# Kernel tuning notes

Measured on AMD Instinct MI355X. Metric: run time of the kernel, lower is better.

Reference implementation:

```python
import jax, jax.numpy as jnp
import numpy as np

N, D = 8192, 64


def setup_inputs() -> dict:
    key = jax.random.key(0)
    k1, k2, k3 = jax.random.split(key, 3)
    X = jax.random.normal(k1, (N, D), dtype=jnp.float32)
    target = jax.random.normal(k2, (N,), dtype=jnp.float32)
    params = jax.random.uniform(k3, (D,), dtype=jnp.float32)  # positive ARD weights
    return {"X": X, "target": target, "params": params}


def reference(X, target, params):
    # ARD-RBF kernel: k(x, y) = exp(-sum(params * (x - y)^2))
    # = exp(-||xs - ys||^2) with xs = x * sqrt(params)
    Xs = X * jnp.sqrt(params)  # [N, D]
    sq = jnp.sum(Xs * Xs, axis=-1)  # [N]
    d2 = jnp.maximum(sq[:, None] + sq[None, :] - 2.0 * (Xs @ Xs.T), 0.0)  # [N, N]
    K = jnp.exp(-d2)
    # torch version initializes K = eye(N) and never overwrites the diagonal
    n = X.shape[0]
    K = K.at[jnp.arange(n), jnp.arange(n)].set(1.0)
    K_target = jnp.outer(target, target)  # [N, N]
    kta = jnp.sum(K * K_target) / (n * jnp.sqrt(jnp.sum(K * K)))
    return -kta
```

## Files before the change

### kernel.cpp

```cpp
#include <hip/hip_runtime.h>
#include <hip/hip_bf16.h>

#define NROWS 8192
#define DIM 64
#define NT 64
#define NTRI (NT * (NT + 1) / 2)

typedef __attribute__((ext_vector_type(8))) short short8;
typedef __attribute__((ext_vector_type(4))) float f32x4;

static constexpr float LOG2E = 1.4426950408889634f;

#if defined(__has_builtin) && __has_builtin(__builtin_amdgcn_exp2f)
#define EXP2F(x) __builtin_amdgcn_exp2f(x)
#else
#define EXP2F(x) exp2f(x)
#endif

__global__ __launch_bounds__(256) void prep_kernel(const float* __restrict__ X,
                                                   const float* __restrict__ params,
                                                   float* __restrict__ Lsq,
                                                   short* __restrict__ Xp) {
    int tid  = threadIdx.x;
    int wave = tid >> 6, lane = tid & 63;
    int r8 = lane >> 3, c = lane & 7;
    int row = blockIdx.x * 32 + wave * 8 + r8;

    const float* xr = X + row * DIM + c * 8;
    float4 x0 = *(const float4*)xr;
    float4 x1 = *(const float4*)(xr + 4);
    float4 p0 = *(const float4*)(params + c * 8);
    float4 p1 = *(const float4*)(params + c * 8 + 4);

    float v[8];
    v[0] = x0.x * sqrtf(p0.x); v[1] = x0.y * sqrtf(p0.y);
    v[2] = x0.z * sqrtf(p0.z); v[3] = x0.w * sqrtf(p0.w);
    v[4] = x1.x * sqrtf(p1.x); v[5] = x1.y * sqrtf(p1.y);
    v[6] = x1.z * sqrtf(p1.z); v[7] = x1.w * sqrtf(p1.w);

    short8 h;
    float s = 0.f;
    #pragma unroll
    for (int i = 0; i < 8; ++i) {
        __hip_bfloat16 b = __float2bfloat16(v[i]);
        union { __hip_bfloat16 bb; short ss; } u; u.bb = b;
        h[i] = u.ss;
        float bf = __bfloat162float(b);
        s += bf * bf;
    }

    int panel = row >> 4, pr = row & 15;
    ((short8*)Xp)[panel * 128 + c * 16 + pr] = h;

    #pragma unroll
    for (int m = 1; m < 8; m <<= 1) s += __shfl_xor(s, m, 64);
    if (c == 0) Lsq[row] = LOG2E * s;
}

__global__ __launch_bounds__(256, 3) void kta_main(const short* __restrict__ Xp,
                                                   const float* __restrict__ Lsq,
                                                   const float* __restrict__ t,
                                                   float2* __restrict__ partial) {
    int k = blockIdx.x;
    int it = (int)((129.0f - sqrtf(16641.0f - 8.0f * (float)k)) * 0.5f);
    if (it > NT - 1) it = NT - 1;
    while ((it * (129 - it)) / 2 > k) --it;
    while (((it + 1) * (128 - it)) / 2 <= k) ++it;
    int jt = it + (k - (it * (129 - it)) / 2);

    int tid  = threadIdx.x;
    int wave = tid >> 6, lane = tid & 63;
    int quad = lane >> 4, l16 = lane & 15;

    __shared__ short8 As[1024];
    __shared__ short8 Bs[1024];

    const short8* Xpv  = (const short8*)Xp;
    const short8* Asrc = Xpv + (size_t)it * 1024;
    const short8* Bsrc = Xpv + (size_t)jt * 1024;

    #pragma unroll
    for (int i = 0; i < 4; ++i) {
        As[tid + i * 256] = Asrc[tid + i * 256];
        Bs[tid + i * 256] = Bsrc[tid + i * 256];
    }

    int rbase = it * 128 + (wave >> 1) * 64;
    int cbase = jt * 128 + (wave & 1) * 64;

    float LsqR[4][4], tR[4][4];
    #pragma unroll
    for (int rt = 0; rt < 4; ++rt)
        #pragma unroll
        for (int r = 0; r < 4; ++r) {
            int row = rbase + rt * 16 + quad * 4 + r;
            LsqR[rt][r] = Lsq[row];
            tR[rt][r]   = t[row];
        }
    float LsqC[4], tC[4];
    #pragma unroll
    for (int ct = 0; ct < 4; ++ct) {
        int col = cbase + ct * 16 + l16;
        LsqC[ct] = Lsq[col];
        tC[ct]   = t[col];
    }

    __syncthreads();

    int lpA = (wave >> 1) * 4;
    int lpB = (wave & 1) * 4;

    short8 bfr[4][2];
    #pragma unroll
    for (int ct = 0; ct < 4; ++ct)
        #pragma unroll
        for (int kc = 0; kc < 2; ++kc)
            bfr[ct][kc] = Bs[(lpB + ct) * 128 + (kc * 4 + quad) * 16 + l16];

    bool diagwave = (it == jt) && ((wave >> 1) == (wave & 1));
    float s1 = 0.f, s2a = 0.f, s2b = 0.f;

    auto body = [&](int DIAG) {
        #pragma unroll
        for (int rt = 0; rt < 4; ++rt) {
            short8 a0 = As[(lpA + rt) * 128 + quad * 16 + l16];
            short8 a1 = As[(lpA + rt) * 128 + (4 + quad) * 16 + l16];
            f32x4 cc[4];
            #pragma unroll
            for (int ct = 0; ct < 4; ++ct) {
                cc[ct] = (f32x4){0.f, 0.f, 0.f, 0.f};
                cc[ct] = __builtin_amdgcn_mfma_f32_16x16x32_bf16(a0, bfr[ct][0], cc[ct], 0, 0, 0);
                cc[ct] = __builtin_amdgcn_mfma_f32_16x16x32_bf16(a1, bfr[ct][1], cc[ct], 0, 0, 0);
            }
            #pragma unroll
            for (int r = 0; r < 4; ++r) {
                float nr = LsqR[rt][r];
                float s1row = 0.f;
                #pragma unroll
                for (int ct = 0; ct < 4; ++ct) {
                    float dot = cc[ct][r];
                    float K = EXP2F(fmaf(dot, 2.0f * LOG2E, -(nr + LsqC[ct])));
                    if (DIAG && (rt == ct) && ((quad * 4 + r) == l16))
                        K = 1.0f;
                    s1row = fmaf(K, tC[ct], s1row);
                    if (ct & 2) s2b = fmaf(K, K, s2b);
                    else        s2a = fmaf(K, K, s2a);
                }
                s1 = fmaf(s1row, tR[rt][r], s1);
            }
        }
    };
    if (diagwave) body(1); else body(0);

    float s2 = s2a + s2b;
    float w = (it == jt) ? 1.0f : 2.0f;
    s1 *= w; s2 *= w;
    #pragma unroll
    for (int m = 32; m > 0; m >>= 1) {
        s1 += __shfl_xor(s1, m, 64);
        s2 += __shfl_xor(s2, m, 64);
    }

    __shared__ float2 red[4];
    if (lane == 0) red[wave] = make_float2(s1, s2);
    __syncthreads();
    if (tid == 0) {
        float2 a = red[0], b = red[1], cc = red[2], d = red[3];
        partial[k] = make_float2(a.x + b.x + cc.x + d.x, a.y + b.y + cc.y + d.y);
    }
}

__global__ __launch_bounds__(256) void finalize_kernel(const float2* __restrict__ partial,
                                                       float* __restrict__ out) {
    float s1 = 0.f, s2 = 0.f;
    for (int i = threadIdx.x; i < NTRI; i += 256) {
        float2 p = partial[i];
        s1 += p.x;
        s2 += p.y;
    }
    #pragma unroll
    for (int m = 32; m > 0; m >>= 1) {
        s1 += __shfl_xor(s1, m, 64);
        s2 += __shfl_xor(s2, m, 64);
    }
    __shared__ float r1[4], r2[4];
    int wave = threadIdx.x >> 6, lane = threadIdx.x & 63;
    if (lane == 0) { r1[wave] = s1; r2[wave] = s2; }
    __syncthreads();
    if (threadIdx.x == 0) {
        float a = r1[0] + r1[1] + r1[2] + r1[3];
        float b = r2[0] + r2[1] + r2[2] + r2[3];
        out[0] = -a / ((float)NROWS * sqrtf(b));
    }
}

extern "C" void kernel_launch(void* const* d_in, const int* in_sizes, int n_in,
                              void* d_out, int out_size, void* d_ws, size_t ws_size,
                              hipStream_t stream) {
    const float* X      = (const float*)d_in[0];
    const float* target = (const float*)d_in[1];
    const float* params = (const float*)d_in[2];
    float* out = (float*)d_out;

    float* ws = (float*)d_ws;
    float2* partial = (float2*)ws;
    float* Lsq = ws + 8192;
    short* Xp  = (short*)(ws + 16384);

    prep_kernel<<<NROWS / 32, 256, 0, stream>>>(X, params, Lsq, Xp);
    kta_main<<<NTRI, 256, 0, stream>>>(Xp, Lsq, target, partial);
    finalize_kernel<<<1, 256, 0, stream>>>(partial, out);
}
```

Before: 74.88 us.

## Fuse prep kernel into main kernel by staging scaled bf16 tiles in-block

```diff
diff --git a/kernel.cpp b/kernel.cpp
--- a/kernel.cpp
+++ b/kernel.cpp
@@ -17,48 +17,8 @@
 #define EXP2F(x) exp2f(x)
 #endif
 
-__global__ __launch_bounds__(256) void prep_kernel(const float* __restrict__ X,
+__global__ __launch_bounds__(256, 3) void kta_main(const float* __restrict__ X,
                                                    const float* __restrict__ params,
-                                                   float* __restrict__ Lsq,
-                                                   short* __restrict__ Xp) {
-    int tid  = threadIdx.x;
-    int wave = tid >> 6, lane = tid & 63;
-    int r8 = lane >> 3, c = lane & 7;
-    int row = blockIdx.x * 32 + wave * 8 + r8;
-
-    const float* xr = X + row * DIM + c * 8;
-    float4 x0 = *(const float4*)xr;
-    float4 x1 = *(const float4*)(xr + 4);
-    float4 p0 = *(const float4*)(params + c * 8);
-    float4 p1 = *(const float4*)(params + c * 8 + 4);
-
-    float v[8];
-    v[0] = x0.x * sqrtf(p0.x); v[1] = x0.y * sqrtf(p0.y);
-    v[2] = x0.z * sqrtf(p0.z); v[3] = x0.w * sqrtf(p0.w);
-    v[4] = x1.x * sqrtf(p1.x); v[5] = x1.y * sqrtf(p1.y);
-    v[6] = x1.z * sqrtf(p1.z); v[7] = x1.w * sqrtf(p1.w);
-
-    short8 h;
-    float s = 0.f;
-    #pragma unroll
-    for (int i = 0; i < 8; ++i) {
-        __hip_bfloat16 b = __float2bfloat16(v[i]);
-        union { __hip_bfloat16 bb; short ss; } u; u.bb = b;
-        h[i] = u.ss;
-        float bf = __bfloat162float(b);
-        s += bf * bf;
-    }
-
-    int panel = row >> 4, pr = row & 15;
-    ((short8*)Xp)[panel * 128 + c * 16 + pr] = h;
-
-    #pragma unroll
-    for (int m = 1; m < 8; m <<= 1) s += __shfl_xor(s, m, 64);
-    if (c == 0) Lsq[row] = LOG2E * s;
-}
-
-__global__ __launch_bounds__(256, 3) void kta_main(const short* __restrict__ Xp,
-                                                   const float* __restrict__ Lsq,
                                                    const float* __restrict__ t,
                                                    float2* __restrict__ partial) {
     int k = blockIdx.x;
@@ -71,53 +31,92 @@
     int tid  = threadIdx.x;
     int wave = tid >> 6, lane = tid & 63;
     int quad = lane >> 4, l16 = lane & 15;
+    int r8 = lane >> 3, ch = lane & 7;
 
     __shared__ short8 As[1024];
     __shared__ short8 Bs[1024];
-
-    const short8* Xpv  = (const short8*)Xp;
-    const short8* Asrc = Xpv + (size_t)it * 1024;
-    const short8* Bsrc = Xpv + (size_t)jt * 1024;
-
-    #pragma unroll
-    for (int i = 0; i < 4; ++i) {
-        As[tid + i * 256] = Asrc[tid + i * 256];
-        Bs[tid + i * 256] = Bsrc[tid + i * 256];
-    }
+    __shared__ float  LA[128];
+    __shared__ float  LB[128];
+
+    float4 p0 = *(const float4*)(params + ch * 8);
+    float4 p1 = *(const float4*)(params + ch * 8 + 4);
+    float sp[8];
+    sp[0] = sqrtf(p0.x); sp[1] = sqrtf(p0.y); sp[2] = sqrtf(p0.z); sp[3] = sqrtf(p0.w);
+    sp[4] = sqrtf(p1.x); sp[5] = sqrtf(p1.y); sp[6] = sqrtf(p1.z); sp[7] = sqrtf(p1.w);
+
+    auto stage = [&](int rowbase, short8* __restrict__ S, float* __restrict__ L) {
+        #pragma unroll
+        for (int pass = 0; pass < 4; ++pass) {
+            int rl = pass * 32 + wave * 8 + r8;
+            const float* xr = X + (size_t)(rowbase + rl) * DIM + ch * 8;
+            float4 x0 = *(const float4*)xr;
+            float4 x1 = *(const float4*)(xr + 4);
+            float v[8];
+            v[0] = x0.x * sp[0]; v[1] = x0.y * sp[1];
+            v[2] = x0.z * sp[2]; v[3] = x0.w * sp[3];
+            v[4] = x1.x * sp[4]; v[5] = x1.y * sp[5];
+            v[6] = x1.z * sp[6]; v[7] = x1.w * sp[7];
+            short8 h;
+            float s = 0.f;
+            #pragma unroll
+            for (int i = 0; i < 8; ++i) {
+                __hip_bfloat16 b = __float2bfloat16(v[i]);
+                union { __hip_bfloat16 bb; short ss; } u; u.bb = b;
+                h[i] = u.ss;
+                float bf = __bfloat162float(b);
+                s = fmaf(bf, bf, s);
+            }
+            S[(rl >> 4) * 128 + ch * 16 + (rl & 15)] = h;
+            #pragma unroll
+            for (int m = 1; m < 8; m <<= 1) s += __shfl_xor(s, m, 64);
+            if (ch == 0) L[rl] = LOG2E * s;
+        }
+    };
+
+    bool diag = (it == jt);
+    stage(it * 128, As, LA);
+    if (!diag) stage(jt * 128, Bs, LB);
+    const short8* Bsel = diag ? As : Bs;
+    const float*  LBsl = diag ? LA : LB;
 
     int rbase = it * 128 + (wave >> 1) * 64;
     int cbase = jt * 128 + (wave & 1) * 64;
 
-    float LsqR[4][4], tR[4][4];
+    float tR[4][4];
     #pragma unroll
     for (int rt = 0; rt < 4; ++rt)
         #pragma unroll
-        for (int r = 0; r < 4; ++r) {
-            int row = rbase + rt * 16 + quad * 4 + r;
-            LsqR[rt][r] = Lsq[row];
-            tR[rt][r]   = t[row];
-        }
-    float LsqC[4], tC[4];
-    #pragma unroll
-    for (int ct = 0; ct < 4; ++ct) {
-        int col = cbase + ct * 16 + l16;
-        LsqC[ct] = Lsq[col];
-        tC[ct]   = t[col];
-    }
+        for (int r = 0; r < 4; ++r)
+            tR[rt][r] = t[rbase + rt * 16 + quad * 4 + r];
+    float tC[4];
+    #pragma unroll
+    for (int ct = 0; ct < 4; ++ct)
+        tC[ct] = t[cbase + ct * 16 + l16];
 
     __syncthreads();
 
     int lpA = (wave >> 1) * 4;
     int lpB = (wave & 1) * 4;
 
+    float LsqR[4][4];
+    #pragma unroll
+    for (int rt = 0; rt < 4; ++rt)
+        #pragma unroll
+        for (int r = 0; r < 4; ++r)
+            LsqR[rt][r] = LA[(wave >> 1) * 64 + rt * 16 + quad * 4 + r];
+    float LsqC[4];
+    #pragma unroll
+    for (int ct = 0; ct < 4; ++ct)
+        LsqC[ct] = LBsl[(wave & 1) * 64 + ct * 16 + l16];
+
     short8 bfr[4][2];
     #pragma unroll
     for (int ct = 0; ct < 4; ++ct)
         #pragma unroll
         for (int kc = 0; kc < 2; ++kc)
-            bfr[ct][kc] = Bs[(lpB + ct) * 128 + (kc * 4 + quad) * 16 + l16];
-
-    bool diagwave = (it == jt) && ((wave >> 1) == (wave & 1));
+            bfr[ct][kc] = Bsel[(lpB + ct) * 128 + (kc * 4 + quad) * 16 + l16];
+
+    bool diagwave = diag && ((wave >> 1) == (wave & 1));
     float s1 = 0.f, s2a = 0.f, s2b = 0.f;
 
     auto body = [&](int DIAG) {
@@ -153,7 +152,7 @@
     if (diagwave) body(1); else body(0);
 
     float s2 = s2a + s2b;
-    float w = (it == jt) ? 1.0f : 2.0f;
+    float w = diag ? 1.0f : 2.0f;
     s1 *= w; s2 *= w;
     #pragma unroll
     for (int m = 32; m > 0; m >>= 1) {
@@ -204,10 +203,7 @@
 
     float* ws = (float*)d_ws;
     float2* partial = (float2*)ws;
-    float* Lsq = ws + 8192;
-    short* Xp  = (short*)(ws + 16384);
-
-    prep_kernel<<<NROWS / 32, 256, 0, stream>>>(X, params, Lsq, Xp);
-    kta_main<<<NTRI, 256, 0, stream>>>(Xp, Lsq, target, partial);
+
+    kta_main<<<NTRI, 256, 0, stream>>>(X, params, target, partial);
     finalize_kernel<<<1, 256, 0, stream>>>(partial, out);
 }
```

Result: slower. 81.62 us (+9.0%).
